# Kernel tuning notes

Measured on AMD Instinct MI355X. Metric: run time of the kernel, lower is better.

## Reference

```python
import jax, jax.numpy as jnp
import numpy as np

ALPHA = 0.12
BETA = 0.88
OMEGA = 6.0
PHI_BASE = 0.0
B, T, D = 4, 4096, 2048


def setup_inputs() -> dict:
    key = jax.random.key(0)
    k1, = jax.random.split(key, 1)
    x = jax.random.normal(k1, (B, T, D), dtype=jnp.float32)
    gate = jnp.asarray(-2.0, dtype=jnp.float32)          # nn.Parameter gate_init
    input_scale = jnp.asarray(4.0, dtype=jnp.float32)     # nn.Parameter init 4.0
    mem_state = jnp.zeros((1, 1, D), dtype=jnp.float32)   # persistent buffer
    return {"x": x, "gate": gate, "input_scale": input_scale,
            "mem_state": mem_state, "step_idx": 0}


def reference(x, gate, input_scale, mem_state, step_idx):
    Bn, Tn, Dn = x.shape
    dtype = x.dtype
    # EMA recurrence: m_t = beta * m_{t-1} + alpha * input_scale * x_t
    u = (ALPHA * input_scale) * x                         # [B,T,D]
    m0 = jnp.broadcast_to(mem_state[:, 0, :], (Bn, Dn))   # [B,D]

    def step(m, u_t):
        m = BETA * m + u_t
        return m, m

    _, ms = jax.lax.scan(step, m0, jnp.swapaxes(u, 0, 1))  # [T,B,D]
    ms = jnp.swapaxes(ms, 0, 1)                            # [B,T,D]

    # log-periodic phase rotation per step (scalar angle per t)
    t_glob = jnp.arange(1, Tn + 1, dtype=dtype) + jnp.asarray(step_idx, dtype)
    theta = (OMEGA * jnp.log1p(t_glob) + PHI_BASE) % (2.0 * jnp.pi)  # [T]
    c = jnp.cos(theta)[None, :, None]
    s = jnp.sin(theta)[None, :, None]
    half = Dn // 2  # D even -> no tail
    a = ms[..., :half]
    b = ms[..., half:2 * half]
    m_rot = jnp.concatenate([a * c - b * s, a * s + b * c], axis=-1)  # [B,T,D]

    # residual gated output: y = x + sigmoid(gate) * m_seq
    return x + jax.nn.sigmoid(gate) * m_rot
```

## Files before the change

kernel.cpp:

```cpp
#include <hip/hip_runtime.h>
#include <math.h>

#define ALPHA 0.12f
#define BETA  0.88f
#define OMEGA 6.0f
#define TWO_PI 6.28318530717958647692f

constexpr int Bn   = 4;
constexpr int Tn   = 4096;
constexpr int Dn   = 2048;
constexpr int HALF = Dn / 2;
constexpr int G    = 16;
constexpr int NQ   = Tn / G;

typedef float fx4 __attribute__((ext_vector_type(4)));

constexpr float beta_pow(int n) {
    float r = 1.0f;
    for (int i = 0; i < n; ++i) r *= BETA;
    return r;
}
constexpr float BETA_G = beta_pow(G);

__global__ __launch_bounds__(256) void k_sub(
        const float* __restrict__ x,
        const float* __restrict__ input_scale,
        float* __restrict__ S) {
    int gid = blockIdx.x * blockDim.x + threadIdx.x;
    int d4 = gid & (Dn / 4 - 1);
    int q  = (gid >> 9) & (NQ - 1);
    int b  = gid >> 17;
    const float sc = ALPHA * (*input_scale);

    const fx4* xp = (const fx4*)(x + ((size_t)b * Tn + (size_t)q * G) * Dn) + d4;
    fx4 m = (fx4)(0.0f);
#pragma unroll
    for (int i = 0; i < G; ++i) {
        fx4 v = xp[(size_t)i * (Dn / 4)];
        m = BETA * m + sc * v;
    }
    ((fx4*)S)[gid] = m;
}

__global__ __launch_bounds__(256) void k_carry(
        float* __restrict__ S,
        const float* __restrict__ mem_state) {
    int gid = blockIdx.x * blockDim.x + threadIdx.x;
    int d4 = gid & (Dn / 4 - 1);
    int b  = gid >> 9;

    fx4 m = ((const fx4*)mem_state)[d4];
    fx4* Sp = (fx4*)S + (size_t)b * NQ * (Dn / 4) + d4;
    for (int q = 0; q < NQ; ++q) {
        fx4 s = Sp[(size_t)q * (Dn / 4)];
        Sp[(size_t)q * (Dn / 4)] = m;
        m = BETA_G * m + s;
    }
}
__global__ __launch_bounds__(256) void k_final(
        const float* __restrict__ x,
        const float* __restrict__ gate,
        const float* __restrict__ input_scale,
        const float* __restrict__ S,
        const int*   __restrict__ step_idx,
        float* __restrict__ out) {
    int p4 = threadIdx.x;
    int q  = blockIdx.x & (NQ - 1);
    int b  = blockIdx.x >> 8;

    const float sc  = ALPHA * (*input_scale);
    const float sig = 1.0f / (1.0f + expf(-(*gate)));

    __shared__ float cs[G];
    __shared__ float ss[G];
    if (threadIdx.x < G) {
        int t = q * G + threadIdx.x;
        float tg = (float)(t + 1 + *step_idx);
        float theta = fmodf(OMEGA * log1pf(tg), TWO_PI);
        cs[threadIdx.x] = cosf(theta);
        ss[threadIdx.x] = sinf(theta);
    }

    const fx4* Fp = (const fx4*)S + (size_t)(b * NQ + q) * (Dn / 4);
    fx4 ma = Fp[p4];
    fx4 mb = Fp[HALF / 4 + p4];
    __syncthreads();

    size_t base = ((size_t)b * Tn + (size_t)q * G) * Dn;
    const fx4* xa = (const fx4*)(x + base) + p4;
    const fx4* xb = (const fx4*)(x + base + HALF) + p4;
    fx4* oa = (fx4*)(out + base) + p4;
    fx4* ob = (fx4*)(out + base + HALF) + p4;

#pragma unroll
    for (int i = 0; i < G; ++i) {
        fx4 va = xa[(size_t)i * (Dn / 4)];
        fx4 vb = xb[(size_t)i * (Dn / 4)];
        ma = BETA * ma + sc * va;
        mb = BETA * mb + sc * vb;
        float cth = cs[i];
        float sth = ss[i];
        fx4 ra = va + sig * (ma * cth - mb * sth);
        fx4 rb = vb + sig * (ma * sth + mb * cth);
        __builtin_nontemporal_store(ra, &oa[(size_t)i * (Dn / 4)]);
        __builtin_nontemporal_store(rb, &ob[(size_t)i * (Dn / 4)]);
    }
}

extern "C" void kernel_launch(void* const* d_in, const int* in_sizes, int n_in,
                              void* d_out, int out_size, void* d_ws, size_t ws_size,
                              hipStream_t stream) {
    const float* x           = (const float*)d_in[0];
    const float* gate        = (const float*)d_in[1];
    const float* input_scale = (const float*)d_in[2];
    const float* mem_state   = (const float*)d_in[3];
    const int*   step_idx    = (const int*)d_in[4];
    float* out = (float*)d_out;

    float* S = (float*)d_ws;

    k_sub<<<(Bn * NQ * Dn / 4) / 256, 256, 0, stream>>>(x, input_scale, S);
    k_carry<<<(Bn * Dn / 4) / 256, 256, 0, stream>>>(S, mem_state);
    k_final<<<Bn * NQ, 256, 0, stream>>>(x, gate, input_scale, S,
                                         step_idx, out);
}
```

Baseline: 282.0 us.

## Replace serial carry kernel with truncated look-back carry in final kernel

Removes the sequential k_carry pass over all chunk summaries. Each block of k_final now rebuilds its incoming EMA state from only the previous LB=6 chunk summaries, weighted by BETA^G, plus mem_state near the start of the sequence. This relies on BETA^(G*LB) being negligible, so the state is an approximation of the exact scan. The block work is split across two blocks with fx2 accesses, and the nontemporal stores become plain stores.

New measurement: 270.4 us. -4.1%, faster.

```diff
diff --git a/kernel.cpp b/kernel.cpp
--- a/kernel.cpp
+++ b/kernel.cpp
@@ -12,7 +12,9 @@
 constexpr int HALF = Dn / 2;
 constexpr int G    = 16;
 constexpr int NQ   = Tn / G;
+constexpr int LB   = 6;
 
+typedef float fx2 __attribute__((ext_vector_type(2)));
 typedef float fx4 __attribute__((ext_vector_type(4)));
 
 constexpr float beta_pow(int n) {
@@ -42,68 +44,70 @@
     ((fx4*)S)[gid] = m;
 }
 
-__global__ __launch_bounds__(256) void k_carry(
-        float* __restrict__ S,
-        const float* __restrict__ mem_state) {
-    int gid = blockIdx.x * blockDim.x + threadIdx.x;
-    int d4 = gid & (Dn / 4 - 1);
-    int b  = gid >> 9;
-
-    fx4 m = ((const fx4*)mem_state)[d4];
-    fx4* Sp = (fx4*)S + (size_t)b * NQ * (Dn / 4) + d4;
-    for (int q = 0; q < NQ; ++q) {
-        fx4 s = Sp[(size_t)q * (Dn / 4)];
-        Sp[(size_t)q * (Dn / 4)] = m;
-        m = BETA_G * m + s;
-    }
-}
 __global__ __launch_bounds__(256) void k_final(
         const float* __restrict__ x,
         const float* __restrict__ gate,
         const float* __restrict__ input_scale,
         const float* __restrict__ S,
+        const float* __restrict__ mem_state,
         const int*   __restrict__ step_idx,
         float* __restrict__ out) {
-    int p4 = threadIdx.x;
-    int q  = blockIdx.x & (NQ - 1);
-    int b  = blockIdx.x >> 8;
+    int tid = threadIdx.x;
+    int h   = blockIdx.x & 1;
+    int q   = (blockIdx.x >> 1) & (NQ - 1);
+    int b   = blockIdx.x >> 9;
 
     const float sc  = ALPHA * (*input_scale);
     const float sig = 1.0f / (1.0f + expf(-(*gate)));
 
     __shared__ float cs[G];
     __shared__ float ss[G];
-    if (threadIdx.x < G) {
-        int t = q * G + threadIdx.x;
+    if (tid < G) {
+        int t = q * G + tid;
         float tg = (float)(t + 1 + *step_idx);
         float theta = fmodf(OMEGA * log1pf(tg), TWO_PI);
-        cs[threadIdx.x] = cosf(theta);
-        ss[threadIdx.x] = sinf(theta);
+        cs[tid] = cosf(theta);
+        ss[tid] = sinf(theta);
     }
 
-    const fx4* Fp = (const fx4*)S + (size_t)(b * NQ + q) * (Dn / 4);
-    fx4 ma = Fp[p4];
-    fx4 mb = Fp[HALF / 4 + p4];
+    int k  = h * 256 + tid;
+    int da = 2 * k;
+
+    fx2 Ea, Eb;
+    int j0 = q - LB;
+    if (j0 < 0) {
+        j0 = 0;
+        Ea = *(const fx2*)(mem_state + da);
+        Eb = *(const fx2*)(mem_state + HALF + da);
+    } else {
+        Ea = (fx2)(0.0f);
+        Eb = (fx2)(0.0f);
+    }
+    const float* Sb_ = S + (size_t)b * NQ * Dn;
+    for (int j = j0; j < q; ++j) {
+        fx2 sa = *(const fx2*)(Sb_ + (size_t)j * Dn + da);
+        fx2 sb = *(const fx2*)(Sb_ + (size_t)j * Dn + HALF + da);
+        Ea = BETA_G * Ea + sa;
+        Eb = BETA_G * Eb + sb;
+    }
     __syncthreads();
 
-    size_t base = ((size_t)b * Tn + (size_t)q * G) * Dn;
-    const fx4* xa = (const fx4*)(x + base) + p4;
-    const fx4* xb = (const fx4*)(x + base + HALF) + p4;
-    fx4* oa = (fx4*)(out + base) + p4;
-    fx4* ob = (fx4*)(out + base + HALF) + p4;
-
+    const float* xrow = x   + ((size_t)b * Tn + (size_t)q * G) * Dn;
+    float*       orow = out + ((size_t)b * Tn + (size_t)q * G) * Dn;
 #pragma unroll
     for (int i = 0; i < G; ++i) {
-        fx4 va = xa[(size_t)i * (Dn / 4)];
-        fx4 vb = xb[(size_t)i * (Dn / 4)];
-        ma = BETA * ma + sc * va;
-        mb = BETA * mb + sc * vb;
+        fx2 va = *(const fx2*)(xrow + da);
+        fx2 vb = *(const fx2*)(xrow + HALF + da);
+        Ea = BETA * Ea + sc * va;
+        Eb = BETA * Eb + sc * vb;
         float cth = cs[i];
         float sth = ss[i];
-        fx4 ra = va + sig * (ma * cth - mb * sth);
-        fx4 rb = vb + sig * (ma * sth + mb * cth);
-        __builtin_nontemporal_store(ra, &oa[(size_t)i * (Dn / 4)]);
-        __builtin_nontemporal_store(rb, &ob[(size_t)i * (Dn / 4)]);
+        fx2 ra = va + sig * (Ea * cth - Eb * sth);
+        fx2 rb = vb + sig * (Ea * sth + Eb * cth);
+        *(fx2*)(orow + da)        = ra;
+        *(fx2*)(orow + HALF + da) = rb;
+        xrow += Dn;
+        orow += Dn;
     }
 }
 
@@ -120,7 +124,6 @@
     float* S = (float*)d_ws;
 
     k_sub<<<(Bn * NQ * Dn / 4) / 256, 256, 0, stream>>>(x, input_scale, S);
-    k_carry<<<(Bn * Dn / 4) / 256, 256, 0, stream>>>(S, mem_state);
-    k_final<<<Bn * NQ, 256, 0, stream>>>(x, gate, input_scale, S,
-                                         step_idx, out);
+    k_final<<<Bn * NQ * 2, 256, 0, stream>>>(x, gate, input_scale, S,
+                                             mem_state, step_idx, out);
 }
```
